# Optimization experiments

Measured on AMD Instinct MI355X. Metric: run time of the kernel, lower is better.

Reference implementation:

```python
import jax, jax.numpy as jnp
import numpy as np

B, N_TOK, N_ATOM = 1, 1024, 4096
C_S, C_Z, C_ATOM, C_PAIR = 384, 128, 128, 16
N_QUERY, N_KEY = 32, 128
N_BLOCKS = N_ATOM // N_QUERY
EPS = 1e-5


def layer_norm_scale(x, w):
    # LayerNorm with create_offset=False (scale only)
    mu = jnp.mean(x, axis=-1, keepdims=True)
    var = jnp.mean(jnp.square(x - mu), axis=-1, keepdims=True)
    return (x - mu) * jax.lax.rsqrt(var + EPS) * w


def atom_to_token_idx(num_atoms):
    # num_atoms: [N_tok] int -> token index for each atom [N_ATOM]
    ends = jnp.cumsum(num_atoms)
    return jnp.searchsorted(ends, jnp.arange(N_ATOM), side='right')


def setup_inputs() -> dict:
    key = jax.random.key(0)
    ks = jax.random.split(key, 10)
    return {
        'token_mask': jnp.ones((B, N_TOK), jnp.float32),
        'num_atoms_per_token': jnp.full((B, N_TOK), N_ATOM // N_TOK, jnp.int32),
        'cl': jax.random.normal(ks[0], (B, N_ATOM, C_ATOM), jnp.float32),
        'plm': jax.random.normal(ks[1], (B, N_BLOCKS, N_QUERY, N_KEY, C_PAIR), jnp.float32),
        'si_trunk': jax.random.normal(ks[2], (B, N_TOK, C_S), jnp.float32),
        'zij_trunk': jax.random.normal(ks[3], (B, N_TOK, N_TOK, C_Z), jnp.float32),
        'rl': jax.random.normal(ks[4], (B, N_ATOM, 3), jnp.float32),
        'ln_s_w': jnp.ones((C_S,), jnp.float32),
        'W_s': jax.random.normal(ks[5], (C_S, C_ATOM), jnp.float32) * 0.02,
        'b_s': jnp.zeros((C_ATOM,), jnp.float32),
        'ln_z_w': jnp.ones((C_Z,), jnp.float32),
        'W_z': jax.random.normal(ks[6], (C_Z, C_PAIR), jnp.float32) * 0.02,
        'b_z': jnp.zeros((C_PAIR,), jnp.float32),
        'W_r': jax.random.normal(ks[7], (3, C_ATOM), jnp.float32) * 0.02,
        'b_r': jnp.zeros((C_ATOM,), jnp.float32),
        'n_query': N_QUERY,
        'n_key': N_KEY,
    }


def reference(token_mask, num_atoms_per_token, cl, plm, si_trunk, zij_trunk, rl,
              ln_s_w, W_s, b_s, ln_z_w, W_z, b_z, W_r, b_r, n_query, n_key):
    # --- single rep: LayerNorm + Linear, then token -> atom broadcast ---
    s = jnp.einsum('btc,cd->btd', layer_norm_scale(si_trunk, ln_s_w), W_s) + b_s
    s = s * token_mask[..., None]  # zero padded tokens
    tok = jax.vmap(atom_to_token_idx)(num_atoms_per_token)  # [B, N_ATOM]
    s_atoms = jnp.take_along_axis(s, tok[..., None], axis=1)  # [B, N_ATOM, c_atom]
    cl_out = cl + s_atoms

    # --- pair rep: LayerNorm + Linear, then pair -> local block gather ---
    z = jnp.einsum('bijc,cd->bijd', layer_norm_scale(zij_trunk, ln_z_w), W_z) + b_z
    n_blocks = N_ATOM // n_query
    q_idx = jnp.arange(n_blocks)[:, None] * n_query + jnp.arange(n_query)[None, :]
    k_off = n_query // 2 - n_key // 2  # key window centered on query block
    k_idx = jnp.arange(n_blocks)[:, None] * n_query + k_off + jnp.arange(n_key)[None, :]
    valid = ((k_idx >= 0) & (k_idx < N_ATOM)).astype(z.dtype)  # [L, n_key]
    k_idx_c = jnp.clip(k_idx, 0, N_ATOM - 1)
    tok_q = tok[:, q_idx]    # [B, L, n_query]
    tok_k = tok[:, k_idx_c]  # [B, L, n_key]

    def gather_blocks(zb, tq, tk):
        return zb[tq[:, :, None], tk[:, None, :]]  # [L, nq, nk, C_PAIR]

    z_blk = jax.vmap(gather_blocks)(z, tok_q, tok_k)
    z_blk = z_blk * valid[None, :, None, :, None]
    plm_out = plm + z_blk

    # --- noisy position projection ---
    ql = cl_out + jnp.einsum('bac,cd->bad', rl, W_r) + b_r
    return cl_out, plm_out, ql
```

## Files before the change

kernel.cpp:

```cpp
#include <hip/hip_runtime.h>

#define N_TOKS 1024
#define N_ATOMS 4096
#define CS 384
#define CZ 128
#define CATOM 128
#define CPAIR 16
#define NQ 32
#define NK 128
#define NBLK 128
#define KOFF (-48)
#define KSEG 32
#define NSEG (NK / KSEG)
#define NTILE (NBLK * NSEG)
#define NB_A 256
#define NB_S (NTILE * 4)
#define MAXP 1024
#define MAPSTRIDE 68
#define LN_EPS 1e-5f

typedef float f32x4 __attribute__((ext_vector_type(4)));

struct alignas(16) SMemB {
    int ends[N_TOKS];
    int tokq[NQ]; int tokk[KSEG];
    int qmap[NQ]; int kmap[KSEG];
    int uqtok[NQ]; int uktok[KSEG];
    int uqk[2];
    int wsum[4];
    int vmask;
};

union alignas(16) SMemS {
    struct {
        int qmap_l[8];
        int kmap_l[32];
        int uk; int vm;
    } s;
    struct {
        float xh[CS][4];
        float sacc[8][4][CATOM];
        float s_l[4][CATOM];
        int ends[N_TOKS];
        int wsum[4];
    } a;
};

__device__ __forceinline__ void scan_ends(const int* __restrict__ na, int* ends, int* wsum, int t) {
    int4 v = ((const int4*)na)[t];
    int e0 = v.x, e1 = e0 + v.y, e2 = e1 + v.z, e3 = e2 + v.w;
    int s = e3;
    int lane = t & 63, w = t >> 6;
    #pragma unroll
    for (int off = 1; off < 64; off <<= 1) {
        int u = __shfl_up(s, off);
        if (lane >= off) s += u;
    }
    if (lane == 63) wsum[w] = s;
    __syncthreads();
    int wbase = 0;
    #pragma unroll
    for (int i = 0; i < 4; i++) wbase += (i < w) ? wsum[i] : 0;
    int base = wbase + s - e3;
    ends[4 * t + 0] = base + e0;
    ends[4 * t + 1] = base + e1;
    ends[4 * t + 2] = base + e2;
    ends[4 * t + 3] = base + e3;
    __syncthreads();
}

__device__ __forceinline__ int bsearch_tok(const int* ends, int a) {
    int lo = 0, hi = N_TOKS - 1;
    while (lo < hi) { int mid = (lo + hi) >> 1; if (ends[mid] > a) hi = mid; else lo = mid + 1; }
    return lo;
}

__global__ __launch_bounds__(256) void k_pre(
        const int* __restrict__ na,
        const float* __restrict__ zij, const float* __restrict__ lnzw,
        const float* __restrict__ Wz, const float* __restrict__ bz,
        float* __restrict__ z_ws, int* __restrict__ maps_ws) {
    __shared__ SMemB sm;
    int t = threadIdx.x;
    int x = blockIdx.x;
    int blk = x >> 2, kseg = x & 3;
    scan_ends(na, sm.ends, sm.wsum, t);

    if (t < NQ) {
        sm.tokq[t] = bsearch_tok(sm.ends, blk * NQ + t);
    } else if (t >= 64 && t < 64 + KSEG) {
        int kk = t - 64;
        int kg = blk * NQ + KOFF + kseg * KSEG + kk;
        unsigned long long vm = __ballot(kg >= 0 && kg < N_ATOMS);
        if (kk == 0) sm.vmask = (int)(vm & 0xffffffffull);
        sm.tokk[kk] = bsearch_tok(sm.ends, min(max(kg, 0), N_ATOMS - 1));
    }
    __syncthreads();

    if (t < NQ) {
        int tq = sm.tokq[t];
        bool head = (t == 0) || (tq != sm.tokq[t - 1]);
        unsigned long long m = __ballot(head);
        int rank = (int)__popcll(m & ((2ull << t) - 1)) - 1;
        sm.qmap[t] = rank;
        if (head) sm.uqtok[rank] = tq;
        if (t == 0) sm.uqk[0] = (int)__popcll(m);
    } else if (t >= 64 && t < 64 + KSEG) {
        int lane = t - 64;
        int tk = sm.tokk[lane];
        bool head = (lane == 0) || (tk != sm.tokk[lane - 1]);
        unsigned long long m = __ballot(head);
        int rank = (int)__popcll(m & ((2ull << lane) - 1)) - 1;
        sm.kmap[lane] = rank;
        if (head) sm.uktok[rank] = tk;
        if (lane == 0) sm.uqk[1] = (int)__popcll(m);
    }
    __syncthreads();
    int uq = sm.uqk[0], uk = sm.uqk[1];
    int npairs = uq * uk;

    int* mp = maps_ws + x * MAPSTRIDE;
    if (t < NQ) mp[1 + t] = sm.qmap[t];
    else if (t >= 64 && t < 64 + KSEG) mp[33 + (t - 64)] = sm.kmap[t - 64];
    else if (t == 96) mp[0] = uk;
    else if (t == 97) mp[65] = sm.vmask;

    for (int p = t; p < npairs; p += 256) {
        int qi = p / uk, ki = p - qi * uk;
        int tq = sm.uqtok[qi], tk = sm.uktok[ki];
        const float* row = zij + ((size_t)tq * N_TOKS + tk) * CZ;
        float sum = 0.f, sq = 0.f;
        for (int c4 = 0; c4 < CZ / 4; c4++) {
            float4 v = *(const float4*)(row + c4 * 4);
            sum += v.x + v.y + v.z + v.w;
            sq  += v.x * v.x + v.y * v.y + v.z * v.z + v.w * v.w;
        }
        float mu = sum * (1.f / CZ);
        float rstd = rsqrtf(sq * (1.f / CZ) - mu * mu + LN_EPS);
        float acc[CPAIR];
        #pragma unroll
        for (int d = 0; d < CPAIR; d++) acc[d] = bz[d];
        for (int c4 = 0; c4 < CZ / 4; c4++) {
            float4 v = *(const float4*)(row + c4 * 4);
            float xs4[4] = {v.x, v.y, v.z, v.w};
            #pragma unroll
            for (int j = 0; j < 4; j++) {
                int c = c4 * 4 + j;
                float xv = (xs4[j] - mu) * rstd * lnzw[c];
                const float* wrow = Wz + c * CPAIR;
                #pragma unroll
                for (int d = 0; d < CPAIR; d++) acc[d] += xv * wrow[d];
            }
        }
        float4* zt = (float4*)(z_ws + ((size_t)x * MAXP + p) * CPAIR);
        zt[0] = make_float4(acc[0], acc[1], acc[2], acc[3]);
        zt[1] = make_float4(acc[4], acc[5], acc[6], acc[7]);
        zt[2] = make_float4(acc[8], acc[9], acc[10], acc[11]);
        zt[3] = make_float4(acc[12], acc[13], acc[14], acc[15]);
    }
}

__global__ __launch_bounds__(256) void k_stream(
        const float* __restrict__ z_ws, const int* __restrict__ maps_ws,
        const float* __restrict__ plm, float* __restrict__ plm_out,
        const int* __restrict__ na, const float* __restrict__ si,
        const float* __restrict__ lnw, const float* __restrict__ Ws,
        const float* __restrict__ bs, const float* __restrict__ mask,
        const float* __restrict__ cl, const float* __restrict__ rl,
        const float* __restrict__ Wr, const float* __restrict__ br,
        float* __restrict__ cl_out, float* __restrict__ ql) {
    __shared__ SMemS sm;
    int t = threadIdx.x;
    int x = blockIdx.x;

    if (x >= NB_S) {
        int b = x - NB_S, Tlo = b * 4;
        scan_ends(na, sm.a.ends, sm.a.wsum, t);
        {
            int tl = t >> 6, l = t & 63;
            const float4* row4 = (const float4*)(si + (size_t)(Tlo + tl) * CS);
            float4 v0 = row4[l];
            float4 v1 = make_float4(0.f, 0.f, 0.f, 0.f);
            if (l < 32) v1 = row4[64 + l];
            float sum = v0.x + v0.y + v0.z + v0.w + v1.x + v1.y + v1.z + v1.w;
            float sq = v0.x*v0.x + v0.y*v0.y + v0.z*v0.z + v0.w*v0.w
                     + v1.x*v1.x + v1.y*v1.y + v1.z*v1.z + v1.w*v1.w;
            #pragma unroll
            for (int m = 32; m >= 1; m >>= 1) { sum += __shfl_xor(sum, m); sq += __shfl_xor(sq, m); }
            float mu = sum * (1.f / CS);
            float rstd = rsqrtf(sq * (1.f / CS) - mu * mu + LN_EPS);
            float4 g0 = ((const float4*)lnw)[l];
            sm.a.xh[4*l+0][tl] = (v0.x - mu) * rstd * g0.x;
            sm.a.xh[4*l+1][tl] = (v0.y - mu) * rstd * g0.y;
            sm.a.xh[4*l+2][tl] = (v0.z - mu) * rstd * g0.z;
            sm.a.xh[4*l+3][tl] = (v0.w - mu) * rstd * g0.w;
            if (l < 32) {
                float4 g1 = ((const float4*)lnw)[64 + l];
                sm.a.xh[256+4*l+0][tl] = (v1.x - mu) * rstd * g1.x;
                sm.a.xh[256+4*l+1][tl] = (v1.y - mu) * rstd * g1.y;
                sm.a.xh[256+4*l+2][tl] = (v1.z - mu) * rstd * g1.z;
                sm.a.xh[256+4*l+3][tl] = (v1.w - mu) * rstd * g1.w;
            }
        }
        __syncthreads();
        {
            int d4 = t & 31, cc = t >> 5;
            float4 a0 = make_float4(0,0,0,0), a1 = a0, a2 = a0, a3 = a0;
            const float4* Ws4 = (const float4*)Ws;
            int c0 = 48 * cc;
            #pragma unroll 4
            for (int c = c0; c < c0 + 48; c++) {
                float4 w = Ws4[(size_t)c * 32 + d4];
                float4 xv = *(const float4*)&sm.a.xh[c][0];
                a0.x += xv.x * w.x; a0.y += xv.x * w.y; a0.z += xv.x * w.z; a0.w += xv.x * w.w;
                a1.x += xv.y * w.x; a1.y += xv.y * w.y; a1.z += xv.y * w.z; a1.w += xv.y * w.w;
                a2.x += xv.z * w.x; a2.y += xv.z * w.y; a2.z += xv.z * w.z; a2.w += xv.z * w.w;
                a3.x += xv.w * w.x; a3.y += xv.w * w.y; a3.z += xv.w * w.z; a3.w += xv.w * w.w;
            }
            *(float4*)&sm.a.sacc[cc][0][d4 * 4] = a0;
            *(float4*)&sm.a.sacc[cc][1][d4 * 4] = a1;
            *(float4*)&sm.a.sacc[cc][2][d4 * 4] = a2;
            *(float4*)&sm.a.sacc[cc][3][d4 * 4] = a3;
        }
        __syncthreads();
        if (t < 128) {
            int tk = t >> 5, d = t & 31;
            float4 a = make_float4(0,0,0,0);
            #pragma unroll
            for (int cc = 0; cc < 8; cc++) {
                float4 p = *(const float4*)&sm.a.sacc[cc][tk][d * 4];
                a.x += p.x; a.y += p.y; a.z += p.z; a.w += p.w;
            }
            float4 bb = ((const float4*)bs)[d];
            float m = mask[Tlo + tk];
            a.x = (a.x + bb.x) * m; a.y = (a.y + bb.y) * m;
            a.z = (a.z + bb.z) * m; a.w = (a.w + bb.w) * m;
            *(float4*)&sm.a.s_l[tk][d * 4] = a;
        }
        __syncthreads();
        int elo = (Tlo == 0) ? 0 : sm.a.ends[Tlo - 1];
        int e_0 = sm.a.ends[Tlo], e_1 = sm.a.ends[Tlo + 1], e_2 = sm.a.ends[Tlo + 2];
        int ehi = (b == NB_A - 1) ? N_ATOMS : sm.a.ends[Tlo + 3];
        elo = min(max(elo, 0), N_ATOMS);
        ehi = min(max(ehi, 0), N_ATOMS);
        if (ehi < elo) ehi = elo;
        int items = (ehi - elo) * 32;
        for (int i = t; i < items; i += 256) {
            int a = elo + (i >> 5), d = i & 31;
            int tk = (a >= e_0) + (a >= e_1) + (a >= e_2);
            float4 c4 = ((const float4*)cl)[(size_t)a * 32 + d];
            float4 sv = *(const float4*)&sm.a.s_l[tk][d * 4];
            float4 co;
            co.x = c4.x + sv.x; co.y = c4.y + sv.y; co.z = c4.z + sv.z; co.w = c4.w + sv.w;
            float px = rl[a * 3 + 0], py = rl[a * 3 + 1], pz = rl[a * 3 + 2];
            float4 w0 = ((const float4*)Wr)[d];
            float4 w1 = ((const float4*)Wr)[32 + d];
            float4 w2 = ((const float4*)Wr)[64 + d];
            float4 bb = ((const float4*)br)[d];
            float4 q;
            q.x = co.x + px * w0.x + py * w1.x + pz * w2.x + bb.x;
            q.y = co.y + px * w0.y + py * w1.y + pz * w2.y + bb.y;
            q.z = co.z + px * w0.z + py * w1.z + pz * w2.z + bb.z;
            q.w = co.w + px * w0.w + py * w1.w + pz * w2.w + bb.w;
            ((float4*)cl_out)[(size_t)a * 32 + d] = co;
            ((float4*)ql)[(size_t)a * 32 + d] = q;
        }
        return;
    }

    int tau = x >> 2, qq = x & 3;
    int blk = tau >> 2, kseg = tau & 3;

    const int* mp = maps_ws + tau * MAPSTRIDE;
    if (t < 32) sm.s.kmap_l[t] = mp[33 + t];
    else if (t < 40) sm.s.qmap_l[t - 32] = mp[1 + qq * 8 + (t - 32)];
    else if (t == 40) sm.s.uk = mp[0];
    else if (t == 41) sm.s.vm = mp[65];
    __syncthreads();
    int uk = sm.s.uk, vm = sm.s.vm;

    const f32x4* plm4 = (const f32x4*)plm;
    const float4* z4 = (const float4*)z_ws;
    f32x4* out4 = (f32x4*)plm_out;

    size_t gs[4];
    f32x4 pv[4];
    #pragma unroll
    for (int i = 0; i < 4; i++) {
        int f = t + i * 256;
        int d4 = f & 3;
        int kk = (f >> 2) & 31;
        int q  = f >> 7;
        int grow = blk * NQ + qq * 8 + q;
        gs[i] = ((size_t)grow * NK + kseg * KSEG + kk) * 4 + d4;
        pv[i] = __builtin_nontemporal_load(&plm4[gs[i]]);
    }
    #pragma unroll
    for (int i = 0; i < 4; i++) {
        int f = t + i * 256;
        int d4 = f & 3;
        int kk = (f >> 2) & 31;
        int q  = f >> 7;
        int pidx = sm.s.qmap_l[q] * uk + sm.s.kmap_l[kk];
        float4 z = z4[((size_t)tau * MAXP + pidx) * 4 + d4];
        float vd = ((vm >> kk) & 1) ? 1.0f : 0.0f;
        f32x4 v = pv[i];
        v.x += vd * z.x; v.y += vd * z.y; v.z += vd * z.z; v.w += vd * z.w;
        __builtin_nontemporal_store(v, &out4[gs[i]]);
    }
}

extern "C" void kernel_launch(void* const* d_in, const int* in_sizes, int n_in,
                              void* d_out, int out_size, void* d_ws, size_t ws_size,
                              hipStream_t stream) {
    (void)in_sizes; (void)n_in; (void)out_size; (void)ws_size;
    const float* token_mask = (const float*)d_in[0];
    const int*   num_atoms  = (const int*)d_in[1];
    const float* cl   = (const float*)d_in[2];
    const float* plm  = (const float*)d_in[3];
    const float* si   = (const float*)d_in[4];
    const float* zij  = (const float*)d_in[5];
    const float* rl   = (const float*)d_in[6];
    const float* ln_s_w = (const float*)d_in[7];
    const float* W_s  = (const float*)d_in[8];
    const float* b_s  = (const float*)d_in[9];
    const float* ln_z_w = (const float*)d_in[10];
    const float* W_z  = (const float*)d_in[11];
    const float* b_z  = (const float*)d_in[12];
    const float* W_r  = (const float*)d_in[13];
    const float* b_r  = (const float*)d_in[14];

    float* out_cl  = (float*)d_out;
    float* out_plm = out_cl + (size_t)N_ATOMS * CATOM;
    float* out_ql  = out_plm + (size_t)NBLK * NQ * NK * CPAIR;

    float* z_ws    = (float*)d_ws;
    int*   maps_ws = (int*)((char*)d_ws + (size_t)NTILE * MAXP * CPAIR * 4);

    k_pre<<<NTILE, 256, 0, stream>>>(num_atoms, zij, ln_z_w, W_z, b_z, z_ws, maps_ws);
    k_stream<<<NB_S + NB_A, 256, 0, stream>>>(z_ws, maps_ws, plm, out_plm,
                                              num_atoms, si, ln_s_w, W_s, b_s, token_mask,
                                              cl, rl, W_r, b_r, out_cl, out_ql);
}
```

Baseline: 40.66 us.

## Restructure pair-gather blocks to cover full key rows and halve projection threads

The pair-scatter blocks are reorganized so each block handles 4 query rows across all 128 keys (8 float4 per thread) instead of 8 queries by a 32-key segment. This halves the number of such blocks and makes each block's plm read and write fully contiguous. Nontemporal loads and stores are replaced with plain ones, and the loads are no longer batched ahead of the gathers. The single-rep projection now uses 128 threads, each reducing 96 channels, which halves the partial-sum buffer but leaves half of each block idle during that step.

Result: slower. 48.37 us (+19.0%).

```diff
diff --git a/kernel.cpp b/kernel.cpp
--- a/kernel.cpp
+++ b/kernel.cpp
@@ -14,12 +14,10 @@
 #define NSEG (NK / KSEG)
 #define NTILE (NBLK * NSEG)
 #define NB_A 256
-#define NB_S (NTILE * 4)
+#define NB_S 1024
 #define MAXP 1024
 #define MAPSTRIDE 68
 #define LN_EPS 1e-5f
-
-typedef float f32x4 __attribute__((ext_vector_type(4)));
 
 struct alignas(16) SMemB {
     int ends[N_TOKS];
@@ -33,15 +31,16 @@
 
 union alignas(16) SMemS {
     struct {
-        int qmap_l[8];
-        int kmap_l[32];
-        int uk; int vm;
+        int kmap_l[NK];
+        int qmap_l[4];
+        int uk_l[4];
+        int vm_l[4];
     } s;
     struct {
+        int ends[N_TOKS];
         float xh[CS][4];
-        float sacc[8][4][CATOM];
+        float sacc[4][4][CATOM];
         float s_l[4][CATOM];
-        int ends[N_TOKS];
         int wsum[4];
     } a;
 };
@@ -203,13 +202,13 @@
             }
         }
         __syncthreads();
-        {
+        if (t < 128) {
             int d4 = t & 31, cc = t >> 5;
             float4 a0 = make_float4(0,0,0,0), a1 = a0, a2 = a0, a3 = a0;
             const float4* Ws4 = (const float4*)Ws;
-            int c0 = 48 * cc;
+            int c0 = 96 * cc;
             #pragma unroll 4
-            for (int c = c0; c < c0 + 48; c++) {
+            for (int c = c0; c < c0 + 96; c++) {
                 float4 w = Ws4[(size_t)c * 32 + d4];
                 float4 xv = *(const float4*)&sm.a.xh[c][0];
                 a0.x += xv.x * w.x; a0.y += xv.x * w.y; a0.z += xv.x * w.z; a0.w += xv.x * w.w;
@@ -227,7 +226,7 @@
             int tk = t >> 5, d = t & 31;
             float4 a = make_float4(0,0,0,0);
             #pragma unroll
-            for (int cc = 0; cc < 8; cc++) {
+            for (int cc = 0; cc < 4; cc++) {
                 float4 p = *(const float4*)&sm.a.sacc[cc][tk][d * 4];
                 a.x += p.x; a.y += p.y; a.z += p.z; a.w += p.w;
             }
@@ -268,45 +267,39 @@
         return;
     }
 
-    int tau = x >> 2, qq = x & 3;
-    int blk = tau >> 2, kseg = tau & 3;
-
-    const int* mp = maps_ws + tau * MAPSTRIDE;
-    if (t < 32) sm.s.kmap_l[t] = mp[33 + t];
-    else if (t < 40) sm.s.qmap_l[t - 32] = mp[1 + qq * 8 + (t - 32)];
-    else if (t == 40) sm.s.uk = mp[0];
-    else if (t == 41) sm.s.vm = mp[65];
-    __syncthreads();
-    int uk = sm.s.uk, vm = sm.s.vm;
-
-    const f32x4* plm4 = (const f32x4*)plm;
+    int blk = x >> 3, qo = (x & 7) * 4;
+
+    const int* mp0 = maps_ws + (blk * 4) * MAPSTRIDE;
+    if (t < NK) {
+        int sg = t >> 5, kl = t & 31;
+        sm.s.kmap_l[t] = mp0[sg * MAPSTRIDE + 33 + kl];
+    } else if (t < 132) {
+        sm.s.uk_l[t - 128] = mp0[(t - 128) * MAPSTRIDE + 0];
+    } else if (t < 136) {
+        sm.s.vm_l[t - 132] = mp0[(t - 132) * MAPSTRIDE + 65];
+    } else if (t < 140) {
+        sm.s.qmap_l[t - 136] = mp0[1 + qo + (t - 136)];
+    }
+    __syncthreads();
+
+    const float4* plm4 = (const float4*)plm;
     const float4* z4 = (const float4*)z_ws;
-    f32x4* out4 = (f32x4*)plm_out;
-
-    size_t gs[4];
-    f32x4 pv[4];
+    float4* out4 = (float4*)plm_out;
+    size_t base = ((size_t)(blk * NQ + qo)) * NK * 4;
+
     #pragma unroll
-    for (int i = 0; i < 4; i++) {
+    for (int i = 0; i < 8; i++) {
         int f = t + i * 256;
         int d4 = f & 3;
-        int kk = (f >> 2) & 31;
-        int q  = f >> 7;
-        int grow = blk * NQ + qq * 8 + q;
-        gs[i] = ((size_t)grow * NK + kseg * KSEG + kk) * 4 + d4;
-        pv[i] = __builtin_nontemporal_load(&plm4[gs[i]]);
-    }
-    #pragma unroll
-    for (int i = 0; i < 4; i++) {
-        int f = t + i * 256;
-        int d4 = f & 3;
-        int kk = (f >> 2) & 31;
-        int q  = f >> 7;
-        int pidx = sm.s.qmap_l[q] * uk + sm.s.kmap_l[kk];
-        float4 z = z4[((size_t)tau * MAXP + pidx) * 4 + d4];
-        float vd = ((vm >> kk) & 1) ? 1.0f : 0.0f;
-        f32x4 v = pv[i];
+        int kk = (f >> 2) & 127;
+        int q  = f >> 9;
+        int sg = kk >> 5, kl = kk & 31;
+        float4 v = plm4[base + f];
+        int pidx = sm.s.qmap_l[q] * sm.s.uk_l[sg] + sm.s.kmap_l[kk];
+        float4 z = z4[((size_t)(blk * 4 + sg) * MAXP + pidx) * 4 + d4];
+        float vd = ((sm.s.vm_l[sg] >> kl) & 1) ? 1.0f : 0.0f;
         v.x += vd * z.x; v.y += vd * z.y; v.z += vd * z.z; v.w += vd * z.w;
-        __builtin_nontemporal_store(v, &out4[gs[i]]);
+        out4[base + f] = v;
     }
 }
 
```
